# Kernel optimization log

Hardware: AMD Instinct MI355X
Metric: run time of the kernel (lower is better)

## Reference

```python
import jax, jax.numpy as jnp
import numpy as np

B, T, C, H = 2, 2048, 1024, 16
DH = C // H
EPS = 1e-5


def _rotary(t_len, d_head):
    inv_freq = 1.0 / (10000.0 ** (jnp.arange(0, d_head, 2, dtype=jnp.float32) / d_head))
    t = jnp.arange(t_len, dtype=jnp.float32)
    freqs = t[:, None] * inv_freq[None, :]           # [T, dh/2]
    emb = jnp.concatenate([freqs, freqs], axis=-1)    # [T, dh]
    return jnp.cos(emb), jnp.sin(emb)


def _apply_rope(x, cos, sin):
    # x: [B,H,T,dh]; cos/sin: [T,dh]
    d = x.shape[-1]
    x1, x2 = x[..., : d // 2], x[..., d // 2 :]
    x_rot = jnp.concatenate([-x2, x1], axis=-1)
    return x * cos + x_rot * sin


def _decay_mask(t_len, n_head):
    gammas = 1.0 - 2.0 ** (-5.0 - jnp.arange(n_head, dtype=jnp.float32))  # [H]
    n = jnp.arange(t_len)[:, None]
    m = jnp.arange(t_len)[None, :]
    dist = n - m
    decay = gammas[:, None, None] ** jnp.maximum(dist, 0).astype(jnp.float32)
    return jnp.where(dist[None] >= 0, decay, 0.0)  # [H,T,T]


def setup_inputs() -> dict:
    key = jax.random.key(0)
    ks = jax.random.split(key, 7)
    s = 1.0 / np.sqrt(C)
    return {
        "x": jax.random.normal(ks[0], (B, T, C), dtype=jnp.float32),
        "Wq": jax.random.normal(ks[1], (C, C), dtype=jnp.float32) * s,
        "Wk": jax.random.normal(ks[2], (C, C), dtype=jnp.float32) * s,
        "Wv": jax.random.normal(ks[3], (C, C), dtype=jnp.float32) * s,
        "Wo": jax.random.normal(ks[4], (C, C), dtype=jnp.float32) * s,
        "gn_weight": jnp.ones((C,), dtype=jnp.float32),
        "gn_bias": jnp.zeros((C,), dtype=jnp.float32),
    }


def reference(x, Wq, Wk, Wv, Wo, gn_weight, gn_bias):
    b, t, c = x.shape
    # projections (torch Linear: y = x @ W.T), split heads -> [B,H,T,dh]
    def proj(W):
        return jnp.einsum("btc,oc->bto", x, W).reshape(b, t, H, DH).transpose(0, 2, 1, 3)
    q, k, v = proj(Wq), proj(Wk), proj(Wv)

    cos, sin = _rotary(t, DH)
    q = _apply_rope(q, cos, sin)
    k = _apply_rope(k, cos, sin)

    decay = _decay_mask(t, H)                          # [H,T,T]
    qk = jnp.einsum("bhtd,bhsd->bhts", q, k) * (1.0 / np.sqrt(DH))
    qk = qk * decay[None]
    out = jnp.einsum("bhts,bhsd->bhtd", qk, v)         # [B,H,T,dh]

    # GroupNorm with n_head groups over channels, per token
    out = out.transpose(0, 2, 1, 3)                    # [B,T,H,dh]
    mu = jnp.mean(out, axis=-1, keepdims=True)
    var = jnp.mean((out - mu) ** 2, axis=-1, keepdims=True)
    out = (out - mu) * jax.lax.rsqrt(var + EPS)
    out = out * gn_weight.reshape(H, DH) + gn_bias.reshape(H, DH)

    out = out.reshape(b, t, c)
    return jnp.einsum("btc,oc->bto", out, Wo)
```

## Files before the change

kernel.cpp:

```cpp
#include <hip/hip_runtime.h>
#include <stdint.h>

#define B_ 2
#define T_ 2048
#define C_ 1024
#define H_ 16
#define DH_ 64
#define M_ (B_*T_)

typedef short bhalf8 __attribute__((ext_vector_type(8)));
typedef float floatx4 __attribute__((ext_vector_type(4)));

__device__ __forceinline__ short f2bf(float f) {
  unsigned u = __float_as_uint(f);
  u += 0x7fffu + ((u >> 16) & 1u);
  return (short)(u >> 16);
}
__device__ __forceinline__ float bf2f(short s) {
  return __uint_as_float(((unsigned)(unsigned short)s) << 16);
}

__device__ __forceinline__ void gll16(void* lds_dst, const void* g_src) {
  __builtin_amdgcn_global_load_lds(
      reinterpret_cast<const uint32_t __attribute__((address_space(1)))*>(
          reinterpret_cast<uintptr_t>(g_src)),
      reinterpret_cast<uint32_t __attribute__((address_space(3)))*>(
          reinterpret_cast<uintptr_t>(lds_dst)),
      16, 0, 0);
}

__global__ void cvt_all(
    const float* __restrict__ x,  const float* __restrict__ wq,
    const float* __restrict__ wk, const float* __restrict__ wv,
    const float* __restrict__ wo,
    short* __restrict__ xb, short* __restrict__ wqb, short* __restrict__ wkb,
    short* __restrict__ wvb, short* __restrict__ wob)
{
  int i = blockIdx.x * blockDim.x + threadIdx.x;
  const float* s; short* d; int off;
  if (i < (M_*C_/4)) { s = x; d = xb; off = i; }
  else {
    int j = i - M_*C_/4;
    int w = j >> 18;
    off = j & ((1<<18) - 1);
    s = (w==0) ? wq : (w==1) ? wk : (w==2) ? wv : wo;
    d = (w==0) ? wqb : (w==1) ? wkb : (w==2) ? wvb : wob;
  }
  float4 v = ((const float4*)s)[off];
  short4 o;
  o.x = f2bf(v.x); o.y = f2bf(v.y); o.z = f2bf(v.z); o.w = f2bf(v.w);
  ((short4*)d)[off] = o;
}

__global__ __launch_bounds__(256) void gemm_qkv(
    const short* __restrict__ X,
    const short* __restrict__ Wq, const short* __restrict__ Wk, const short* __restrict__ Wv,
    short* __restrict__ Qb, short* __restrict__ Kb, short* __restrict__ Vt)
{
  __shared__ __align__(16) short As[2][128*32];
  __shared__ __align__(16) short Bs[2][128*32];
  const int tid  = threadIdx.x;
  const int lane = tid & 63;
  const int wv   = tid >> 6;
  const int l15  = lane & 15;
  const int quad = lane >> 4;
  const int wm   = (wv >> 1) << 6;
  const int wn   = (wv & 1) << 6;
  const int nx   = blockIdx.x;
  const int m0   = blockIdx.y << 7;
  const int K    = C_;

  const short *Ab, *Bb;
  int nloc, kind;
  if (nx < 8)       { kind = 0; nloc = nx << 7;        Ab = X  + (size_t)m0*K;   Bb = Wq + (size_t)nloc*K; }
  else if (nx < 16) { kind = 1; nloc = (nx - 8) << 7;  Ab = X  + (size_t)m0*K;   Bb = Wk + (size_t)nloc*K; }
  else              { kind = 2; nloc = (nx - 16) << 7; Ab = Wv + (size_t)nloc*K; Bb = X  + (size_t)m0*K;   }

  auto stage = [&](int buf, int k0) {
#pragma unroll
    for (int i = 0; i < 2; ++i) {
      int pA = (i<<8) + tid;
      int r = pA >> 2, go = (pA & 3) ^ ((r >> 1) & 3);
      gll16(&As[buf][((i<<8) + (wv<<6))*8], Ab + (size_t)r*K + k0 + (go<<3));
      gll16(&Bs[buf][((i<<8) + (wv<<6))*8], Bb + (size_t)r*K + k0 + (go<<3));
    }
  };

  floatx4 acc[4][4] = {};
  stage(0, 0);
  int cur = 0;
  for (int it = 0; it < 32; ++it) {
    __syncthreads();
    if (it < 31) stage(cur ^ 1, (it + 1) << 5);
    bhalf8 af[4], bfr[4];
#pragma unroll
    for (int rt = 0; rt < 4; ++rt) {
      int row = wm + rt*16 + l15;
      af[rt] = *(const bhalf8*)&As[cur][(row<<5) + ((quad ^ ((row>>1)&3))<<3)];
    }
#pragma unroll
    for (int ct = 0; ct < 4; ++ct) {
      int row = wn + ct*16 + l15;
      bfr[ct] = *(const bhalf8*)&Bs[cur][(row<<5) + ((quad ^ ((row>>1)&3))<<3)];
    }
#pragma unroll
    for (int rt = 0; rt < 4; ++rt)
#pragma unroll
      for (int ct = 0; ct < 4; ++ct)
        acc[rt][ct] = __builtin_amdgcn_mfma_f32_16x16x32_bf16(af[rt], bfr[ct], acc[rt][ct], 0, 0, 0);
    cur ^= 1;
  }

  if (kind < 2) {
    short* Cb = kind ? Kb : Qb;
    const int hh = (nloc + wn) >> 6;
#pragma unroll
    for (int rt = 0; rt < 4; ++rt)
#pragma unroll
      for (int r = 0; r < 4; ++r) {
        int n  = m0 + wm + rt*16 + quad*4 + r;
        int bb = n >> 11, t = n & (T_-1);
        size_t base = ((size_t)(bb*H_ + hh)*T_ + t)*DH_;
        float tf = (float)t;
#pragma unroll
        for (int ct = 0; ct < 2; ++ct) {
          int ii = ct*16 + l15;
          float ang = tf * exp2f((float)ii * (-0.4152410118609203f));
          float sn = __sinf(ang), cs = __cosf(ang);
          float xlo = acc[rt][ct][r], xhi = acc[rt][ct+2][r];
          Cb[base + ii]      = f2bf(xlo*cs - xhi*sn);
          Cb[base + ii + 32] = f2bf(xhi*cs + xlo*sn);
        }
      }
  } else {
#pragma unroll
    for (int rt = 0; rt < 4; ++rt)
#pragma unroll
      for (int r = 0; r < 4; ++r) {
        int o = nloc + wm + rt*16 + quad*4 + r;
#pragma unroll
        for (int ct = 0; ct < 4; ++ct) {
          int n  = m0 + wn + ct*16 + l15;
          int bb = n >> 11, t = n & (T_-1);
          Vt[(size_t)bb*(C_*T_) + (size_t)o*T_ + t] = f2bf(acc[rt][ct][r]);
        }
      }
  }
}

__global__ __launch_bounds__(256) void gemm_out(
    const short* __restrict__ A, const short* __restrict__ Bm, float* __restrict__ Cf)
{
  __shared__ __align__(16) short As[2][128*32];
  __shared__ __align__(16) short Bs[2][64*32];
  const int tid = threadIdx.x, lane = tid & 63, wv = tid >> 6;
  const int l15 = lane & 15, quad = lane >> 4;
  const int n0 = blockIdx.x << 6;
  const int m0 = blockIdx.y << 7;

  const short* Ab = A  + (size_t)m0 * C_;
  const short* Bb = Bm + (size_t)n0 * C_;

  auto stage = [&](int buf, int k0) {
#pragma unroll
    for (int i = 0; i < 2; ++i) {
      int p = (i<<8) + tid, r = p >> 2, go = (p & 3) ^ ((r >> 1) & 3);
      gll16(&As[buf][((i<<8) + (wv<<6))*8], Ab + (size_t)r*C_ + k0 + (go<<3));
    }
    {
      int p = tid, r = p >> 2, go = (p & 3) ^ ((r >> 1) & 3);
      gll16(&Bs[buf][(wv<<6)*8], Bb + (size_t)r*C_ + k0 + (go<<3));
    }
  };

  floatx4 acc[2][4] = {};
  stage(0, 0);
  int cur = 0;
  for (int it = 0; it < 32; ++it) {
    __syncthreads();
    if (it < 31) stage(cur ^ 1, (it + 1) << 5);
    bhalf8 af[2], bfr[4];
#pragma unroll
    for (int rt = 0; rt < 2; ++rt) {
      int row = (wv<<5) + rt*16 + l15;
      af[rt] = *(const bhalf8*)&As[cur][(row<<5) + ((quad ^ ((row>>1)&3))<<3)];
    }
#pragma unroll
    for (int ct = 0; ct < 4; ++ct) {
      int row = ct*16 + l15;
      bfr[ct] = *(const bhalf8*)&Bs[cur][(row<<5) + ((quad ^ ((row>>1)&3))<<3)];
    }
#pragma unroll
    for (int rt = 0; rt < 2; ++rt)
#pragma unroll
      for (int ct = 0; ct < 4; ++ct)
        acc[rt][ct] = __builtin_amdgcn_mfma_f32_16x16x32_bf16(af[rt], bfr[ct], acc[rt][ct], 0, 0, 0);
    cur ^= 1;
  }

#pragma unroll
  for (int rt = 0; rt < 2; ++rt)
#pragma unroll
    for (int r = 0; r < 4; ++r) {
      int n = m0 + (wv<<5) + rt*16 + quad*4 + r;
#pragma unroll
      for (int ct = 0; ct < 4; ++ct)
        Cf[(size_t)n * C_ + n0 + ct*16 + l15] = acc[rt][ct][r];
    }
}

__global__ __launch_bounds__(256) void transpose_k(
    const short* __restrict__ Kb, short* __restrict__ Kt)
{
  __shared__ short tile[64*66];
  const int idx = blockIdx.x, bh = idx >> 5, tc = idx & 31;
  const int t0 = tc << 6;
  const short* src = Kb + ((size_t)bh*T_ + t0) * DH_;
  int row = threadIdx.x >> 2, c0 = (threadIdx.x & 3) << 4;
  *(int4*)&tile[row*66 + c0]     = *(const int4*)&src[row*64 + c0];
  *(int4*)&tile[row*66 + c0 + 8] = *(const int4*)&src[row*64 + c0 + 8];
  __syncthreads();
  short* dst = Kt + (size_t)bh*DH_*T_;
  int d = threadIdx.x >> 2, k0 = (threadIdx.x & 3) << 4;
  short tmp[16];
#pragma unroll
  for (int i = 0; i < 16; ++i) tmp[i] = tile[(k0 + i)*66 + d];
  *(int4*)&dst[(size_t)d*T_ + t0 + k0]     = *(const int4*)&tmp[0];
  *(int4*)&dst[(size_t)d*T_ + t0 + k0 + 8] = *(const int4*)&tmp[8];
}

__global__ __launch_bounds__(256) void seg_state(
    const short* __restrict__ Kt, const short* __restrict__ Vt,
    short* __restrict__ Pseg)
{
  __shared__ __align__(16) short Ks[2][64*64];
  __shared__ __align__(16) short Vs[2][64*64];
  const int tid = threadIdx.x, lane = tid & 63, wv = tid >> 6;
  const int l15 = lane & 15, quad = lane >> 4;
  const int wrow = wv << 4;
  const int bh = blockIdx.x >> 3, p = blockIdx.x & 7;
  const int h = bh & 15;
  const float log2g = log2f(1.f - exp2f(-5.f - (float)h));
  const float g64 = exp2f(log2g * 64.f);

  float wgt[16];
#pragma unroll
  for (int ks = 0; ks < 2; ++ks)
#pragma unroll
    for (int i = 0; i < 8; ++i)
      wgt[ks*8 + i] = exp2f(log2g * (float)(64 - (ks*32 + (quad<<3) + i)));

  const short* Ktg = Kt + (size_t)bh*DH_*T_;
  const short* Vtg = Vt + (size_t)bh*DH_*T_;

  auto stage = [&](int buf, int jc) {
    const int m0 = ((p<<2) + jc) << 6;
#pragma unroll
    for (int i = 0; i < 2; ++i) {
      int slot = (i<<8) + tid;
      int r = slot >> 3, g = (slot & 7) ^ (r & 7);
      gll16(&Ks[buf][((i<<8) + (wv<<6))*8], Ktg + (size_t)r*T_ + m0 + (g<<3));
      gll16(&Vs[buf][((i<<8) + (wv<<6))*8], Vtg + (size_t)r*T_ + m0 + (g<<3));
    }
  };

  floatx4 acc[4] = {};
  stage(0, 0);
  int cur = 0;
  for (int j = 0; j < 4; ++j) {
    __syncthreads();
    if (j < 3) stage(cur ^ 1, j + 1);
#pragma unroll
    for (int ct = 0; ct < 4; ++ct)
#pragma unroll
      for (int r = 0; r < 4; ++r) acc[ct][r] *= g64;
#pragma unroll
    for (int ks = 0; ks < 2; ++ks) {
      int row = wrow + l15;
      bhalf8 va = *(const bhalf8*)&Vs[cur][(row<<6) + ((((ks<<2)+quad) ^ (row&7))<<3)];
      bhalf8 aw;
#pragma unroll
      for (int i = 0; i < 8; ++i) aw[i] = f2bf(bf2f(va[i]) * wgt[ks*8 + i]);
      bhalf8 bk[4];
#pragma unroll
      for (int ct = 0; ct < 4; ++ct) {
        int kr = ct*16 + l15;
        bk[ct] = *(const bhalf8*)&Ks[cur][(kr<<6) + ((((ks<<2)+quad) ^ (kr&7))<<3)];
      }
#pragma unroll
      for (int ct = 0; ct < 4; ++ct)
        acc[ct] = __builtin_amdgcn_mfma_f32_16x16x32_bf16(aw, bk[ct], acc[ct], 0, 0, 0);
    }
    cur ^= 1;
  }
  size_t base = (size_t)(bh*8 + p) * 2 * 4096;
#pragma unroll
  for (int ct = 0; ct < 4; ++ct)
#pragma unroll
    for (int r = 0; r < 4; ++r) {
      int e = wrow + (quad<<2) + r, d = ct*16 + l15;
      float x = acc[ct][r];
      short hi = f2bf(x);
      short lo = f2bf(x - bf2f(hi));
      Pseg[base + e*64 + d]        = hi;
      Pseg[base + 4096 + e*64 + d] = lo;
    }
}

__global__ __launch_bounds__(256) void retention_chunk(
    const short* __restrict__ Qb, const short* __restrict__ Kb,
    const short* __restrict__ Kt, const short* __restrict__ Vt,
    const short* __restrict__ Pseg,
    const float* __restrict__ gnw, const float* __restrict__ gnb,
    short* __restrict__ Xn)
{
  __shared__ __align__(16) short Vs[64*64];
  __shared__ __align__(16) short Kts[64*64];
  __shared__ __align__(16) short KSs[64*64];
  __shared__ __align__(16) short Sh[64*64];
  __shared__ __align__(16) short Sl[64*64];

  const int tid = threadIdx.x, lane = tid & 63, wv = tid >> 6;
  const int l15 = lane & 15, quad = lane >> 4;
  const int wrow = wv << 4;

  const int idx = blockIdx.x;
  const int bh = idx & 31;
  const int cc = idx >> 5;
  const int c  = ((cc & 7) << 2) | (cc >> 3);
  const int p = c >> 2, j = c & 3;
  const int b = bh >> 4, h = bh & 15;
  const int n0 = c << 6;

  const float log2g = log2f(1.f - exp2f(-5.f - (float)h));
  const float g64 = exp2f(log2g * 64.f);

  const short* Qg  = Qb + ((size_t)bh*T_ + n0 + wrow) * DH_;
  const short* Kg  = Kb + (size_t)bh*T_*DH_;
  const short* Ktg = Kt + (size_t)bh*DH_*T_;
  const short* Vtg = Vt + (size_t)bh*DH_*T_;

  bhalf8 aq[2];
#pragma unroll
  for (int ks = 0; ks < 2; ++ks)
    aq[ks] = *(const bhalf8*)(Qg + (size_t)l15*DH_ + ks*32 + quad*8);

  float rowf[4], colf0[4];
#pragma unroll
  for (int r = 0; r < 4; ++r)
    rowf[r] = exp2f(log2g * (float)(wrow + (quad<<2) + r)) * 0.125f;
#pragma unroll
  for (int ct = 0; ct < 4; ++ct)
    colf0[ct] = exp2f(-log2g * (float)(ct*16 + l15));

  const bool has_state = (c > 0);

  floatx4 st[4] = {};
  if (j > 0) {
    float wgt[16];
#pragma unroll
    for (int ks = 0; ks < 2; ++ks)
#pragma unroll
      for (int i = 0; i < 8; ++i)
        wgt[ks*8 + i] = exp2f(log2g * (float)(64 - (ks*32 + (quad<<3) + i)));
    for (int jp = 0; jp < j; ++jp) {
      if (log2g * (float)((j - 1 - jp) << 6) < -34.f) continue;
      const int m0 = ((p<<2) + jp) << 6;
      __syncthreads();
#pragma unroll
      for (int i = 0; i < 2; ++i) {
        int slot = (i<<8) + tid;
        int r = slot >> 3, g = (slot & 7) ^ (r & 7);
        gll16(&Kts[((i<<8) + (wv<<6))*8], Ktg + (size_t)r*T_ + m0 + (g<<3));
        gll16(&Vs[((i<<8) + (wv<<6))*8],  Vtg + (size_t)r*T_ + m0 + (g<<3));
      }
      __syncthreads();
#pragma unroll
      for (int ct = 0; ct < 4; ++ct)
#pragma unroll
        for (int r = 0; r < 4; ++r) st[ct][r] *= g64;
#pragma unroll
      for (int ks = 0; ks < 2; ++ks) {
        int row = wrow + l15;
        bhalf8 va = *(const bhalf8*)&Vs[(row<<6) + ((((ks<<2)+quad) ^ (row&7))<<3)];
        bhalf8 aw;
#pragma unroll
        for (int i = 0; i < 8; ++i) aw[i] = f2bf(bf2f(va[i]) * wgt[ks*8 + i]);
        bhalf8 bk[4];
#pragma unroll
        for (int ct = 0; ct < 4; ++ct) {
          int kr = ct*16 + l15;
          bk[ct] = *(const bhalf8*)&Kts[(kr<<6) + ((((ks<<2)+quad) ^ (kr&7))<<3)];
        }
#pragma unroll
        for (int ct = 0; ct < 4; ++ct)
          st[ct] = __builtin_amdgcn_mfma_f32_16x16x32_bf16(aw, bk[ct], st[ct], 0, 0, 0);
      }
    }
  }
  for (int pp = 0; pp < p; ++pp) {
    float wexp = log2g * (float)(n0 - ((pp + 1) << 8));
    if (wexp < -34.f) continue;
    float w = exp2f(wexp);
    const short* Pg = Pseg + (size_t)(bh*8 + pp) * 2 * 4096;
#pragma unroll
    for (int ct = 0; ct < 4; ++ct)
#pragma unroll
      for (int r = 0; r < 4; ++r) {
        int e = wrow + (quad<<2) + r, d = ct*16 + l15;
        st[ct][r] += w * (bf2f(Pg[e*64 + d]) + bf2f(Pg[4096 + e*64 + d]));
      }
  }
  if (has_state) {
#pragma unroll
    for (int ct = 0; ct < 4; ++ct)
#pragma unroll
      for (int r = 0; r < 4; ++r) {
        int e = wrow + (quad<<2) + r, d = ct*16 + l15;
        float x = st[ct][r];
        short hi = f2bf(x);
        short lo = f2bf(x - bf2f(hi));
        int addr = (e<<6) + ((((d>>3) ^ (e&7))<<3)) + (d&7);
        Sh[addr] = hi; Sl[addr] = lo;
      }
  }

  __syncthreads();
#pragma unroll
  for (int i = 0; i < 2; ++i) {
    int slot = (i<<8) + tid;
    int r = slot >> 3, g = (slot & 7) ^ (r & 7);
    gll16(&KSs[((i<<8) + (wv<<6))*8], Kg  + (size_t)(n0 + r)*DH_ + (g<<3));
    gll16(&Vs[((i<<8) + (wv<<6))*8],  Vtg + (size_t)r*T_ + n0 + (g<<3));
  }
  __syncthreads();

  floatx4 sacc[4] = {};
#pragma unroll
  for (int ks = 0; ks < 2; ++ks) {
    bhalf8 bk[4];
#pragma unroll
    for (int ct = 0; ct < 4; ++ct) {
      int row = ct*16 + l15;
      bk[ct] = *(const bhalf8*)&KSs[(row<<6) + ((((ks<<2)+quad) ^ (row&7))<<3)];
    }
#pragma unroll
    for (int ct = 0; ct < 4; ++ct)
      sacc[ct] = __builtin_amdgcn_mfma_f32_16x16x32_bf16(aq[ks], bk[ct], sacc[ct], 0, 0, 0);
  }
  __syncthreads();
#pragma unroll
  for (int ct = 0; ct < 4; ++ct) {
    float cf = colf0[ct];
    int colg = (ct<<1) + (l15>>3);
    int m = ct*16 + l15;
#pragma unroll
    for (int r = 0; r < 4; ++r) {
      int row = wrow + (quad<<2) + r;
      float v = (row >= m) ? sacc[ct][r] * (rowf[r] * cf) : 0.f;
      KSs[(row<<6) + ((colg ^ ((row>>1)&7))<<3) + (l15&7)] = f2bf(v);
    }
  }
  floatx4 oacc[4] = {};
#pragma unroll
  for (int ks = 0; ks < 2; ++ks) {
    int row = wrow + l15;
    bhalf8 as_ = *(const bhalf8*)&KSs[(row<<6) + ((((ks<<2)+quad) ^ ((row>>1)&7))<<3)];
    bhalf8 bv[4];
#pragma unroll
    for (int ct = 0; ct < 4; ++ct) {
      int vrow = ct*16 + l15;
      bv[ct] = *(const bhalf8*)&Vs[(vrow<<6) + ((((ks<<2)+quad) ^ (vrow&7))<<3)];
    }
#pragma unroll
    for (int ct = 0; ct < 4; ++ct)
      oacc[ct] = __builtin_amdgcn_mfma_f32_16x16x32_bf16(as_, bv[ct], oacc[ct], 0, 0, 0);
  }

  if (has_state) {
    floatx4 iacc[4] = {};
#pragma unroll
    for (int ks = 0; ks < 2; ++ks) {
      bhalf8 bhf[4], blf[4];
#pragma unroll
      for (int ct = 0; ct < 4; ++ct) {
        int er = ct*16 + l15;
        int ga = ((((ks<<2)+quad) ^ (er&7))<<3);
        bhf[ct] = *(const bhalf8*)&Sh[(er<<6) + ga];
        blf[ct] = *(const bhalf8*)&Sl[(er<<6) + ga];
      }
#pragma unroll
      for (int ct = 0; ct < 4; ++ct) {
        iacc[ct] = __builtin_amdgcn_mfma_f32_16x16x32_bf16(aq[ks], bhf[ct], iacc[ct], 0, 0, 0);
        iacc[ct] = __builtin_amdgcn_mfma_f32_16x16x32_bf16(aq[ks], blf[ct], iacc[ct], 0, 0, 0);
      }
    }
#pragma unroll
    for (int ct = 0; ct < 4; ++ct)
#pragma unroll
      for (int r = 0; r < 4; ++r)
        oacc[ct][r] += rowf[r] * iacc[ct][r];
  }

#pragma unroll
  for (int r = 0; r < 4; ++r) {
    float s1 = oacc[0][r] + oacc[1][r] + oacc[2][r] + oacc[3][r];
    float s2 = oacc[0][r]*oacc[0][r] + oacc[1][r]*oacc[1][r]
             + oacc[2][r]*oacc[2][r] + oacc[3][r]*oacc[3][r];
#pragma unroll
    for (int off = 1; off < 16; off <<= 1) {
      s1 += __shfl_xor(s1, off);
      s2 += __shfl_xor(s2, off);
    }
    float mean = s1 * (1.f/64.f);
    float var  = s2 * (1.f/64.f) - mean*mean;
    float rstd = rsqrtf(var + 1e-5f);
    int t = n0 + wrow + (quad<<2) + r;
    size_t obase = ((size_t)b*T_ + t)*C_ + h*DH_;
#pragma unroll
    for (int ct = 0; ct < 4; ++ct) {
      int d = ct*16 + l15;
      float y = (oacc[ct][r] - mean)*rstd*gnw[h*DH_ + d] + gnb[h*DH_ + d];
      Xn[obase + d] = f2bf(y);
    }
  }
}

extern "C" void kernel_launch(void* const* d_in, const int* in_sizes, int n_in,
                              void* d_out, int out_size, void* d_ws, size_t ws_size,
                              hipStream_t stream) {
  (void)in_sizes; (void)n_in; (void)out_size; (void)ws_size;
  const float* x   = (const float*)d_in[0];
  const float* Wq  = (const float*)d_in[1];
  const float* Wk  = (const float*)d_in[2];
  const float* Wv  = (const float*)d_in[3];
  const float* Wo  = (const float*)d_in[4];
  const float* gnw = (const float*)d_in[5];
  const float* gnb = (const float*)d_in[6];
  float* out = (float*)d_out;

  char* ws = (char*)d_ws;
  short* Xb   = (short*)(ws);
  short* Ktb  = (short*)(ws);
  short* Wqb  = (short*)(ws + (8u<<20));
  short* Pseg = (short*)(ws + (8u<<20));
  short* Wkb  = (short*)(ws + (10u<<20));
  short* Wvb  = (short*)(ws + (12u<<20));
  short* Wob  = (short*)(ws + (14u<<20));
  short* Qb   = (short*)(ws + (16u<<20));
  short* Kb   = (short*)(ws + (24u<<20));
  short* Vtw  = (short*)(ws + (32u<<20));
  short* Xn   = (short*)(ws + (40u<<20));

  cvt_all<<<(M_*C_/4 + 4*(C_*C_/4)) / 256, 256, 0, stream>>>(
      x, Wq, Wk, Wv, Wo, Xb, Wqb, Wkb, Wvb, Wob);

  gemm_qkv<<<dim3(24, 32), 256, 0, stream>>>(Xb, Wqb, Wkb, Wvb, Qb, Kb, Vtw);
  transpose_k<<<1024, 256, 0, stream>>>(Kb, Ktb);
  seg_state<<<256, 256, 0, stream>>>(Ktb, Vtw, Pseg);
  retention_chunk<<<1024, 256, 0, stream>>>(Qb, Kb, Ktb, Vtw, Pseg, gnw, gnb, Xn);
  gemm_out<<<dim3(16, 32), 256, 0, stream>>>(Xn, Wob, out);
}
```

Measured before the change: 175.4 us.

## Rewrite QKV GEMM with 256x256 tiles, 8 waves and phased pipelining

The QKV projection GEMM now uses 256x256 output tiles with BK=64, 512 threads (8 waves) and a single 1D grid of 192 blocks remapped for XCD locality. The main loop is split into four phases that interleave LDS fragment reads, global-to-LDS prefetch of the next buffer, explicit waitcnt/barrier control and setprio around the MFMA bursts. The aim is more data reuse per loaded byte and better overlap of memory and compute. In exchange the kernel uses much more LDS and registers, and 192 blocks may leave some CUs idle.

```diff
diff --git a/kernel.cpp b/kernel.cpp
--- a/kernel.cpp
+++ b/kernel.cpp
@@ -52,97 +52,188 @@
   ((short4*)d)[off] = o;
 }
 
-__global__ __launch_bounds__(256) void gemm_qkv(
+__global__ __launch_bounds__(512, 2) void gemm_qkv(
     const short* __restrict__ X,
     const short* __restrict__ Wq, const short* __restrict__ Wk, const short* __restrict__ Wv,
     short* __restrict__ Qb, short* __restrict__ Kb, short* __restrict__ Vt)
 {
-  __shared__ __align__(16) short As[2][128*32];
-  __shared__ __align__(16) short Bs[2][128*32];
+  __shared__ __align__(16) short As[2][256*64];
+  __shared__ __align__(16) short Bs[2][256*64];
   const int tid  = threadIdx.x;
   const int lane = tid & 63;
-  const int wv   = tid >> 6;
+  const int wid  = tid >> 6;
   const int l15  = lane & 15;
   const int quad = lane >> 4;
-  const int wm   = (wv >> 1) << 6;
-  const int wn   = (wv & 1) << 6;
-  const int nx   = blockIdx.x;
-  const int m0   = blockIdx.y << 7;
+  const int wr   = wid >> 2;
+  const int wc   = wid & 3;
   const int K    = C_;
 
+  const int bid = blockIdx.x;
+  const int wg  = (bid & 7) * 24 + (bid >> 3);
+  const int nx  = wg % 12;
+  const int m0  = (wg / 12) << 8;
+
+  int kind, nloc;
   const short *Ab, *Bb;
-  int nloc, kind;
-  if (nx < 8)       { kind = 0; nloc = nx << 7;        Ab = X  + (size_t)m0*K;   Bb = Wq + (size_t)nloc*K; }
-  else if (nx < 16) { kind = 1; nloc = (nx - 8) << 7;  Ab = X  + (size_t)m0*K;   Bb = Wk + (size_t)nloc*K; }
-  else              { kind = 2; nloc = (nx - 16) << 7; Ab = Wv + (size_t)nloc*K; Bb = X  + (size_t)m0*K;   }
-
-  auto stage = [&](int buf, int k0) {
-#pragma unroll
-    for (int i = 0; i < 2; ++i) {
-      int pA = (i<<8) + tid;
-      int r = pA >> 2, go = (pA & 3) ^ ((r >> 1) & 3);
-      gll16(&As[buf][((i<<8) + (wv<<6))*8], Ab + (size_t)r*K + k0 + (go<<3));
-      gll16(&Bs[buf][((i<<8) + (wv<<6))*8], Bb + (size_t)r*K + k0 + (go<<3));
-    }
+  if (nx < 4)      { kind = 0; nloc = nx << 8;       Ab = X  + (size_t)m0*K;   Bb = Wq + (size_t)nloc*K; }
+  else if (nx < 8) { kind = 1; nloc = (nx - 4) << 8; Ab = X  + (size_t)m0*K;   Bb = Wk + (size_t)nloc*K; }
+  else             { kind = 2; nloc = (nx - 8) << 8; Ab = Wv + (size_t)nloc*K; Bb = X  + (size_t)m0*K;   }
+
+  const int r_loc = tid >> 3;
+  const int g_lin = tid & 7;
+
+  auto stageU = [&](short* lds, const short* g, int q, int k0) {
+    int row = (q << 6) + r_loc;
+    int gs  = g_lin ^ (row & 7);
+    gll16(lds + (q << 12) + (wid << 9), g + (size_t)row * K + k0 + (gs << 3));
   };
 
-  floatx4 acc[4][4] = {};
-  stage(0, 0);
-  int cur = 0;
-  for (int it = 0; it < 32; ++it) {
-    __syncthreads();
-    if (it < 31) stage(cur ^ 1, (it + 1) << 5);
-    bhalf8 af[4], bfr[4];
-#pragma unroll
-    for (int rt = 0; rt < 4; ++rt) {
-      int row = wm + rt*16 + l15;
-      af[rt] = *(const bhalf8*)&As[cur][(row<<5) + ((quad ^ ((row>>1)&3))<<3)];
-    }
-#pragma unroll
-    for (int ct = 0; ct < 4; ++ct) {
-      int row = wn + ct*16 + l15;
-      bfr[ct] = *(const bhalf8*)&Bs[cur][(row<<5) + ((quad ^ ((row>>1)&3))<<3)];
-    }
-#pragma unroll
-    for (int rt = 0; rt < 4; ++rt)
-#pragma unroll
-      for (int ct = 0; ct < 4; ++ct)
-        acc[rt][ct] = __builtin_amdgcn_mfma_f32_16x16x32_bf16(af[rt], bfr[ct], acc[rt][ct], 0, 0, 0);
-    cur ^= 1;
+  floatx4 acc[8][4] = {};
+
+  stageU(&Bs[0][0], Bb, 0, 0); stageU(&Bs[0][0], Bb, 1, 0);
+  stageU(&Bs[0][0], Bb, 2, 0); stageU(&Bs[0][0], Bb, 3, 0);
+  stageU(&As[0][0], Ab, 0, 0); stageU(&As[0][0], Ab, 2, 0);
+  stageU(&As[0][0], Ab, 1, 0); stageU(&As[0][0], Ab, 3, 0);
+  asm volatile("s_waitcnt vmcnt(2)" ::: "memory");
+  __builtin_amdgcn_s_barrier();
+  __builtin_amdgcn_sched_barrier(0);
+
+  for (int t = 0; t < 16; ++t) {
+    const int buf = t & 1, nbuf = buf ^ 1;
+    const int kn = (t + 1) << 6;
+    const bool pf = (t < 15);
+    bhalf8 aF[4], bF[4];
+
+#pragma unroll
+    for (int i = 0; i < 4; ++i) {
+      int row = (wr << 7) + (i << 4) + l15;
+      aF[i] = *(const bhalf8*)&As[buf][(row << 6) + ((quad ^ (row & 7)) << 3)];
+    }
+#pragma unroll
+    for (int n = 0; n < 4; ++n) {
+      int row = (wc << 6) + (n << 4) + l15;
+      bF[n] = *(const bhalf8*)&Bs[buf][(row << 6) + ((quad ^ (row & 7)) << 3)];
+    }
+    if (pf) { stageU(&Bs[nbuf][0], Bb, 0, kn); stageU(&Bs[nbuf][0], Bb, 1, kn); }
+    __builtin_amdgcn_s_barrier();
+    asm volatile("s_waitcnt lgkmcnt(0)" ::: "memory");
+    __builtin_amdgcn_sched_barrier(0);
+    __builtin_amdgcn_s_setprio(1);
+#pragma unroll
+    for (int i = 0; i < 4; ++i)
+#pragma unroll
+      for (int n = 0; n < 4; ++n)
+        acc[i][n] = __builtin_amdgcn_mfma_f32_16x16x32_bf16(aF[i], bF[n], acc[i][n], 0, 0, 0);
+    __builtin_amdgcn_s_setprio(0);
+    asm volatile("s_waitcnt vmcnt(2)" ::: "memory");
+    __builtin_amdgcn_s_barrier();
+    __builtin_amdgcn_sched_barrier(0);
+
+#pragma unroll
+    for (int i = 0; i < 4; ++i) {
+      int row = (wr << 7) + ((4 + i) << 4) + l15;
+      aF[i] = *(const bhalf8*)&As[buf][(row << 6) + ((quad ^ (row & 7)) << 3)];
+    }
+    if (pf) { stageU(&Bs[nbuf][0], Bb, 2, kn); stageU(&Bs[nbuf][0], Bb, 3, kn); }
+    __builtin_amdgcn_s_barrier();
+    asm volatile("s_waitcnt lgkmcnt(0)" ::: "memory");
+    __builtin_amdgcn_sched_barrier(0);
+    __builtin_amdgcn_s_setprio(1);
+#pragma unroll
+    for (int i = 0; i < 4; ++i)
+#pragma unroll
+      for (int n = 0; n < 4; ++n)
+        acc[4 + i][n] = __builtin_amdgcn_mfma_f32_16x16x32_bf16(aF[i], bF[n], acc[4 + i][n], 0, 0, 0);
+    __builtin_amdgcn_s_setprio(0);
+    asm volatile("s_waitcnt vmcnt(4)" ::: "memory");
+    __builtin_amdgcn_s_barrier();
+    __builtin_amdgcn_sched_barrier(0);
+
+#pragma unroll
+    for (int i = 0; i < 4; ++i) {
+      int row = (wr << 7) + (i << 4) + l15;
+      aF[i] = *(const bhalf8*)&As[buf][(row << 6) + (((4 + quad) ^ (row & 7)) << 3)];
+    }
+#pragma unroll
+    for (int n = 0; n < 4; ++n) {
+      int row = (wc << 6) + (n << 4) + l15;
+      bF[n] = *(const bhalf8*)&Bs[buf][(row << 6) + (((4 + quad) ^ (row & 7)) << 3)];
+    }
+    if (pf) { stageU(&As[nbuf][0], Ab, 0, kn); stageU(&As[nbuf][0], Ab, 2, kn); }
+    __builtin_amdgcn_s_barrier();
+    asm volatile("s_waitcnt lgkmcnt(0)" ::: "memory");
+    __builtin_amdgcn_sched_barrier(0);
+    __builtin_amdgcn_s_setprio(1);
+#pragma unroll
+    for (int i = 0; i < 4; ++i)
+#pragma unroll
+      for (int n = 0; n < 4; ++n)
+        acc[i][n] = __builtin_amdgcn_mfma_f32_16x16x32_bf16(aF[i], bF[n], acc[i][n], 0, 0, 0);
+    __builtin_amdgcn_s_setprio(0);
+    asm volatile("s_waitcnt vmcnt(6)" ::: "memory");
+    __builtin_amdgcn_s_barrier();
+    __builtin_amdgcn_sched_barrier(0);
+
+#pragma unroll
+    for (int i = 0; i < 4; ++i) {
+      int row = (wr << 7) + ((4 + i) << 4) + l15;
+      aF[i] = *(const bhalf8*)&As[buf][(row << 6) + (((4 + quad) ^ (row & 7)) << 3)];
+    }
+    if (pf) { stageU(&As[nbuf][0], Ab, 1, kn); stageU(&As[nbuf][0], Ab, 3, kn); }
+    __builtin_amdgcn_s_barrier();
+    asm volatile("s_waitcnt lgkmcnt(0)" ::: "memory");
+    __builtin_amdgcn_sched_barrier(0);
+    __builtin_amdgcn_s_setprio(1);
+#pragma unroll
+    for (int i = 0; i < 4; ++i)
+#pragma unroll
+      for (int n = 0; n < 4; ++n)
+        acc[4 + i][n] = __builtin_amdgcn_mfma_f32_16x16x32_bf16(aF[i], bF[n], acc[4 + i][n], 0, 0, 0);
+    __builtin_amdgcn_s_setprio(0);
+    asm volatile("s_waitcnt vmcnt(2)" ::: "memory");
+    __builtin_amdgcn_s_barrier();
+    __builtin_amdgcn_sched_barrier(0);
   }
 
   if (kind < 2) {
     short* Cb = kind ? Kb : Qb;
-    const int hh = (nloc + wn) >> 6;
-#pragma unroll
-    for (int rt = 0; rt < 4; ++rt)
+    const int hh = (nloc + (wc << 6)) >> 6;
+    const float frq0 = exp2f((float)l15        * (-0.4152410118609203f));
+    const float frq1 = exp2f((float)(l15 + 16) * (-0.4152410118609203f));
+#pragma unroll
+    for (int m = 0; m < 8; ++m)
 #pragma unroll
       for (int r = 0; r < 4; ++r) {
-        int n  = m0 + wm + rt*16 + quad*4 + r;
-        int bb = n >> 11, t = n & (T_-1);
-        size_t base = ((size_t)(bb*H_ + hh)*T_ + t)*DH_;
-        float tf = (float)t;
-#pragma unroll
-        for (int ct = 0; ct < 2; ++ct) {
-          int ii = ct*16 + l15;
-          float ang = tf * exp2f((float)ii * (-0.4152410118609203f));
+        int n  = m0 + (wr << 7) + (m << 4) + (quad << 2) + r;
+        int bb = n >> 11, tt = n & (T_ - 1);
+        size_t base = ((size_t)(bb * H_ + hh) * T_ + tt) * DH_;
+        float tf = (float)tt;
+        {
+          float ang = tf * frq0;
           float sn = __sinf(ang), cs = __cosf(ang);
-          float xlo = acc[rt][ct][r], xhi = acc[rt][ct+2][r];
-          Cb[base + ii]      = f2bf(xlo*cs - xhi*sn);
-          Cb[base + ii + 32] = f2bf(xhi*cs + xlo*sn);
+          float xlo = acc[m][0][r], xhi = acc[m][2][r];
+          Cb[base + l15]      = f2bf(xlo * cs - xhi * sn);
+          Cb[base + l15 + 32] = f2bf(xhi * cs + xlo * sn);
         }
+        {
+          float ang = tf * frq1;
+          float sn = __sinf(ang), cs = __cosf(ang);
+          float xlo = acc[m][1][r], xhi = acc[m][3][r];
+          Cb[base + l15 + 16] = f2bf(xlo * cs - xhi * sn);
+          Cb[base + l15 + 48] = f2bf(xhi * cs + xlo * sn);
+        }
       }
   } else {
 #pragma unroll
-    for (int rt = 0; rt < 4; ++rt)
+    for (int m = 0; m < 8; ++m)
 #pragma unroll
       for (int r = 0; r < 4; ++r) {
-        int o = nloc + wm + rt*16 + quad*4 + r;
-#pragma unroll
-        for (int ct = 0; ct < 4; ++ct) {
-          int n  = m0 + wn + ct*16 + l15;
-          int bb = n >> 11, t = n & (T_-1);
-          Vt[(size_t)bb*(C_*T_) + (size_t)o*T_ + t] = f2bf(acc[rt][ct][r]);
+        int o = nloc + (wr << 7) + (m << 4) + (quad << 2) + r;
+#pragma unroll
+        for (int n = 0; n < 4; ++n) {
+          int tk = m0 + (wc << 6) + (n << 4) + l15;
+          int bb = tk >> 11, tt = tk & (T_ - 1);
+          Vt[(size_t)bb * (C_ * T_) + (size_t)o * T_ + tt] = f2bf(acc[m][n][r]);
         }
       }
   }
@@ -555,7 +646,7 @@
   cvt_all<<<(M_*C_/4 + 4*(C_*C_/4)) / 256, 256, 0, stream>>>(
       x, Wq, Wk, Wv, Wo, Xb, Wqb, Wkb, Wvb, Wob);
 
-  gemm_qkv<<<dim3(24, 32), 256, 0, stream>>>(Xb, Wqb, Wkb, Wvb, Qb, Kb, Vtw);
+  gemm_qkv<<<dim3(192), 512, 0, stream>>>(Xb, Wqb, Wkb, Wvb, Qb, Kb, Vtw);
   transpose_k<<<1024, 256, 0, stream>>>(Kb, Ktb);
   seg_state<<<256, 256, 0, stream>>>(Ktb, Vtw, Pseg);
   retention_chunk<<<1024, 256, 0, stream>>>(Qb, Kb, Ktb, Vtw, Pseg, gnw, gnb, Xn);
```

New measurement: 170.2 us. -2.9%, faster.
